# Optimization experiments

Hardware: AMD Instinct MI355X
Metric: run time of the kernel (lower is better)

Reference implementation:

```python
import jax, jax.numpy as jnp
import numpy as np

S, B, C, H, W, N = 2, 16, 80, 128, 128, 128
HW = H * W
EPS = 1e-4
PULL_W = PUSH_W = OFF_W = 1.0


def _sig(x):
    return jnp.clip(jax.nn.sigmoid(x), EPS, 1.0 - EPS)


def _gather_feat(feat, ind):
    # feat [B,C,H,W], ind [B,N] flat HW indices -> [B,N,C]
    b, c = feat.shape[0], feat.shape[1]
    f = feat.transpose(0, 2, 3, 1).reshape(b, -1, c)
    idx = jnp.broadcast_to(ind[:, :, None], (b, ind.shape[1], c))
    return jnp.take_along_axis(f, idx, axis=1)


def _focal(pred, gt):
    pos = gt == 1.0
    neg = gt < 1.0
    negw = jnp.square(jnp.square(1.0 - gt))  # (1-gt)^4
    pos_loss = jnp.sum(jnp.where(pos, jnp.log(pred) * jnp.square(1.0 - pred), 0.0))
    neg_loss = jnp.sum(jnp.where(neg, jnp.log(1.0 - pred) * jnp.square(pred) * negw, 0.0))
    num_pos = jnp.sum(pos.astype(pred.dtype))
    return jnp.where(num_pos > 0, -(pos_loss + neg_loss) / num_pos, -neg_loss)


def _ae(tag0, tag1, mask):
    t0 = tag0[..., 0]  # [B,N]
    t1 = tag1[..., 0]
    m = mask.astype(t0.dtype)
    num = jnp.sum(m, axis=1, keepdims=True)  # [B,1]
    mean = (t0 + t1) * 0.5
    pull = jnp.sum(m * jnp.square(t0 - mean) / (num + EPS)) + \
           jnp.sum(m * jnp.square(t1 - mean) / (num + EPS))
    m2 = m[:, None, :] * m[:, :, None]  # [B,N,N] both-valid pairs
    numc = num[:, :, None]              # [B,1,1]
    num2 = (numc - 1.0) * numc
    dist = jax.nn.relu(1.0 - jnp.abs(mean[:, None, :] - mean[:, :, None]))
    dist = (dist - 1.0 / (numc + EPS)) / (num2 + EPS)
    push = jnp.sum(m2 * dist)
    return pull, push


def _off_loss(off, gt_off, mask):
    m = mask.astype(off.dtype)
    num = jnp.sum(m)
    d = jnp.abs(off - gt_off)
    sl1 = jnp.where(d < 1.0, 0.5 * d * d, d - 0.5)
    return jnp.sum(m[:, :, None] * sl1) / (num + EPS)


def setup_inputs() -> dict:
    key = jax.random.key(0)
    ks = jax.random.split(key, 20)

    def mk_gt(k):
        k1, k2 = jax.random.split(k)
        base = jax.random.uniform(k1, (B, C * H * W), jnp.float32) * 0.99
        idx = jax.random.randint(k2, (B, 64), 0, C * H * W)
        base = base.at[jnp.arange(B)[:, None], idx].set(1.0)
        return base.reshape(B, C, H, W)

    return {
        "tl_heats": jax.random.normal(ks[0], (S, B, C, H, W), jnp.float32),
        "br_heats": jax.random.normal(ks[1], (S, B, C, H, W), jnp.float32),
        "tl_tags": jax.random.normal(ks[2], (S, B, 1, H, W), jnp.float32),
        "br_tags": jax.random.normal(ks[3], (S, B, 1, H, W), jnp.float32),
        "tl_offs": jax.random.normal(ks[4], (S, B, 2, H, W), jnp.float32),
        "br_offs": jax.random.normal(ks[5], (S, B, 2, H, W), jnp.float32),
        "gt_tl_heat": mk_gt(ks[6]),
        "gt_br_heat": mk_gt(ks[7]),
        "gt_tag_mask": jax.random.bernoulli(ks[8], 0.5, (B, N)),
        "gt_off_tl_mask": jax.random.bernoulli(ks[9], 0.5, (B, N)),
        "gt_off_br_mask": jax.random.bernoulli(ks[10], 0.5, (B, N)),
        "gt_tl_off": jax.random.uniform(ks[11], (B, N, 2), jnp.float32),
        "gt_br_off": jax.random.uniform(ks[12], (B, N, 2), jnp.float32),
        "gt_tl_tag_ind": jax.random.randint(ks[13], (B, N), 0, HW),
        "gt_br_tag_ind": jax.random.randint(ks[14], (B, N), 0, HW),
        "gt_tl_off_ind": jax.random.randint(ks[15], (B, N), 0, HW),
        "gt_br_off_ind": jax.random.randint(ks[16], (B, N), 0, HW),
    }


def reference(tl_heats, br_heats, tl_tags, br_tags, tl_offs, br_offs,
              gt_tl_heat, gt_br_heat, gt_tag_mask, gt_off_tl_mask, gt_off_br_mask,
              gt_tl_off, gt_br_off, gt_tl_tag_ind, gt_br_tag_ind,
              gt_tl_off_ind, gt_br_off_ind):
    nstack = tl_heats.shape[0]
    focal = 0.0
    pull = 0.0
    push = 0.0
    off = 0.0
    for s in range(nstack):
        focal = focal + _focal(_sig(tl_heats[s]), gt_tl_heat)
        focal = focal + _focal(_sig(br_heats[s]), gt_br_heat)
        t0 = _gather_feat(tl_tags[s], gt_tl_tag_ind)
        t1 = _gather_feat(br_tags[s], gt_br_tag_ind)
        p, q = _ae(t0, t1, gt_tag_mask)
        pull = pull + p
        push = push + q
        o0 = _gather_feat(tl_offs[s], gt_tl_off_ind)
        o1 = _gather_feat(br_offs[s], gt_br_off_ind)
        off = off + _off_loss(o0, gt_tl_off, gt_off_tl_mask)
        off = off + _off_loss(o1, gt_br_off, gt_off_br_mask)
    loss = (focal + PULL_W * pull + PUSH_W * push + OFF_W * off) / max(nstack, 1)
    return loss[None]
```

## Files before the change

kernel.cpp:

```cpp
#include <hip/hip_runtime.h>
#include <math.h>

constexpr int S_ = 2, B_ = 16, C_ = 80, H_ = 128, W_ = 128, N_ = 128;
constexpr int HW_ = H_ * W_;
constexpr long long BCHW_ = (long long)B_ * C_ * HW_;
constexpr int NV4_ = (int)(BCHW_ / 4);
#define EPSF 1e-4f

constexpr int FOCAL_BPS = 1024;
constexpr int F4_PER_BLOCK = NV4_ / FOCAL_BPS;
constexpr int F4_PER_THREAD = F4_PER_BLOCK / 256;
constexpr int BATCH = 4;
constexpr int NBATCH = F4_PER_THREAD / BATCH;

#define CLAMP_C 9.2102404f


__device__ inline float wave_reduce_sum(float v) {
#pragma unroll
  for (int off = 32; off > 0; off >>= 1) v += __shfl_down(v, off, 64);
  return v;
}

__device__ inline void focal_elem2(float x, float wpos, float wneg, float negw,
                                   float& pacc, float& nacc) {
  float xc = fminf(fmaxf(-x, -CLAMP_C), CLAMP_C);
  float t = __expf(xc);
  float u = 1.0f + t;
  float p = __builtin_amdgcn_rcpf(u);
  float l1 = __logf(u);
  float om = t * p;
  float posv = l1 * om * om;
  float negv = (l1 - xc) * p * p * negw;
  pacc = fmaf(wpos, posv, pacc);
  nacc = fmaf(wneg, negv, nacc);
}

__device__ inline void focal4(const float4& g, const float4& a, const float4& b,
                              float& pacc, float& nacc, float& npos) {
  const float ge[4] = {g.x, g.y, g.z, g.w};
  const float ae[4] = {a.x, a.y, a.z, a.w};
  const float be[4] = {b.x, b.y, b.z, b.w};
#pragma unroll
  for (int k = 0; k < 4; ++k) {
    const float gv = ge[k];
    const float wpos = (gv == 1.0f) ? 1.0f : 0.0f;
    const float wneg = 1.0f - wpos;
    const float omg = 1.0f - gv;
    const float negw = (omg * omg) * (omg * omg);
    npos += wpos;
    focal_elem2(ae[k], wpos, wneg, negw, pacc, nacc);
    focal_elem2(be[k], wpos, wneg, negw, pacc, nacc);
  }
}

__global__ __launch_bounds__(256, 2) void focal_kernel(
    const float4* __restrict__ tl, const float4* __restrict__ br,
    const float4* __restrict__ gtl, const float4* __restrict__ gbr,
    float* __restrict__ ws) {
  const int slice = blockIdx.y;
  const float4* __restrict__ pred = (slice == 0) ? tl : br;
  const float4* __restrict__ gt = (slice == 0) ? gtl : gbr;

  float pacc = 0.0f, nacc = 0.0f, npos = 0.0f;

  const int idx = blockIdx.x * F4_PER_BLOCK + threadIdx.x;

  float4 bg[2][BATCH], ba[2][BATCH], bb[2][BATCH];

#pragma unroll
  for (int i = 0; i < BATCH; ++i) {
    const int j = idx + i * 256;
    bg[0][i] = gt[j];
    ba[0][i] = pred[j];
    bb[0][i] = pred[NV4_ + j];
  }

#pragma unroll
  for (int bt = 0; bt < NBATCH; ++bt) {
    const int cur = bt & 1, nxt = cur ^ 1;
    if (bt + 1 < NBATCH) {
      const int base = idx + (bt + 1) * (BATCH * 256);
#pragma unroll
      for (int i = 0; i < BATCH; ++i) {
        const int j = base + i * 256;
        bg[nxt][i] = gt[j];
        ba[nxt][i] = pred[j];
        bb[nxt][i] = pred[NV4_ + j];
      }
    }
    __builtin_amdgcn_sched_barrier(0);
#pragma unroll
    for (int i = 0; i < BATCH; ++i) {
      focal4(bg[cur][i], ba[cur][i], bb[cur][i], pacc, nacc, npos);
    }
  }

  __shared__ float red[4][3];
  const int wave = threadIdx.x >> 6, lane = threadIdx.x & 63;
  float r0 = wave_reduce_sum(pacc);
  float r1 = wave_reduce_sum(nacc);
  float r2 = wave_reduce_sum(npos);
  if (lane == 0) { red[wave][0] = r0; red[wave][1] = r1; red[wave][2] = r2; }
  __syncthreads();
  if (threadIdx.x == 0) {
    float tp = red[0][0] + red[1][0] + red[2][0] + red[3][0];
    float tn = red[0][1] + red[1][1] + red[2][1] + red[3][1];
    float tc = red[0][2] + red[1][2] + red[2][2] + red[3][2];
    atomicAdd(&ws[0 + slice], tp);
    atomicAdd(&ws[2 + slice], tn);
    atomicAdd(&ws[4 + slice], tc);
  }
}

__device__ inline float sl1f(float d) {
  float a = fabsf(d);
  return (a < 1.0f) ? 0.5f * a * a : a - 0.5f;
}

__global__ __launch_bounds__(128) void ae_off_kernel(
    const float* __restrict__ tl_tags, const float* __restrict__ br_tags,
    const float* __restrict__ tl_offs, const float* __restrict__ br_offs,
    const int* __restrict__ tag_mask,
    const int* __restrict__ off_tl_mask, const int* __restrict__ off_br_mask,
    const float* __restrict__ gt_tl_off, const float* __restrict__ gt_br_off,
    const int* __restrict__ tl_tag_ind, const int* __restrict__ br_tag_ind,
    const int* __restrict__ tl_off_ind, const int* __restrict__ br_off_ind,
    float* __restrict__ ws, float* __restrict__ out) {
  const int s = blockIdx.x / B_;
  const int b = blockIdx.x % B_;
  const int n = threadIdx.x;

  __shared__ float sm_mean[N_];
  __shared__ float sm_m[N_];

  const float m = (tag_mask[b * N_ + n] != 0) ? 1.0f : 0.0f;
  const float t0 = tl_tags[(s * B_ + b) * HW_ + tl_tag_ind[b * N_ + n]];
  const float t1 = br_tags[(s * B_ + b) * HW_ + br_tag_ind[b * N_ + n]];
  const float mean = 0.5f * (t0 + t1);
  sm_mean[n] = mean;
  sm_m[n] = m;
  __syncthreads();

  float num = 0.0f;
  for (int j = 0; j < N_; ++j) num += sm_m[j];
  const float invn = 1.0f / (num + EPSF);
  const float d0 = t0 - mean, d1 = t1 - mean;
  const float pull_n = m * (d0 * d0 + d1 * d1) * invn;

  const float num2 = (num - 1.0f) * num;
  const float inv2 = 1.0f / (num2 + EPSF);
  float pacc = 0.0f;
  for (int j = 0; j < N_; ++j) {
    float dd = 1.0f - fabsf(mean - sm_mean[j]);
    dd = fmaxf(dd, 0.0f);
    pacc += sm_m[j] * (dd - invn);
  }
  const float push_n = m * pacc * inv2;

  const float mo_tl = (off_tl_mask[b * N_ + n] != 0) ? 1.0f : 0.0f;
  const float mo_br = (off_br_mask[b * N_ + n] != 0) ? 1.0f : 0.0f;
  const int io0 = tl_off_ind[b * N_ + n];
  const int io1 = br_off_ind[b * N_ + n];
  const float o00 = tl_offs[((s * B_ + b) * 2 + 0) * HW_ + io0];
  const float o01 = tl_offs[((s * B_ + b) * 2 + 1) * HW_ + io0];
  const float o10 = br_offs[((s * B_ + b) * 2 + 0) * HW_ + io1];
  const float o11 = br_offs[((s * B_ + b) * 2 + 1) * HW_ + io1];
  const float g00 = gt_tl_off[(b * N_ + n) * 2 + 0];
  const float g01 = gt_tl_off[(b * N_ + n) * 2 + 1];
  const float g10 = gt_br_off[(b * N_ + n) * 2 + 0];
  const float g11 = gt_br_off[(b * N_ + n) * 2 + 1];
  const float sl_tl = mo_tl * (sl1f(o00 - g00) + sl1f(o01 - g01));
  const float sl_br = mo_br * (sl1f(o10 - g10) + sl1f(o11 - g11));

  float vals[6] = {pull_n, push_n, sl_tl, sl_br,
                   (s == 0) ? mo_tl : 0.0f, (s == 0) ? mo_br : 0.0f};
  __shared__ float red[2][6];
  const int wave = n >> 6, lane = n & 63;
#pragma unroll
  for (int k = 0; k < 6; ++k) {
    float r = wave_reduce_sum(vals[k]);
    if (lane == 0) red[wave][k] = r;
  }
  __syncthreads();
  if (n == 0) {
    atomicAdd(&ws[10 + s], red[0][0] + red[1][0]);
    atomicAdd(&ws[12 + s], red[0][1] + red[1][1]);
    atomicAdd(&ws[14 + s], red[0][2] + red[1][2]);
    atomicAdd(&ws[16 + s], red[0][3] + red[1][3]);
    atomicAdd(&ws[18], red[0][4] + red[1][4]);
    atomicAdd(&ws[19], red[0][5] + red[1][5]);

    __threadfence();
    unsigned int prev =
        atomicAdd(reinterpret_cast<unsigned int*>(ws + 31), 1u);
    if (prev == (unsigned int)(S_ * B_ - 1)) {
      auto rd = [&](int i) { return atomicAdd(&ws[i], 0.0f); };
      const float npos_tl = rd(4), npos_br = rd(5);
      float focal = 0.0f;
      const float p_tl = rd(0), n_tl = rd(2);
      const float p_br = rd(1), n_br = rd(3);
      focal += (npos_tl > 0.0f) ? (p_tl + n_tl) / npos_tl : n_tl;
      focal += (npos_br > 0.0f) ? (p_br + n_br) / npos_br : n_br;
      const float pull = rd(10) + rd(11);
      const float push = rd(12) + rd(13);
      const float off = (rd(14) + rd(15)) / (rd(18) + EPSF) +
                        (rd(16) + rd(17)) / (rd(19) + EPSF);
      out[0] = (focal + pull + push + off) * 0.5f;
    }
  }
}

extern "C" void kernel_launch(void* const* d_in, const int* in_sizes, int n_in,
                              void* d_out, int out_size, void* d_ws, size_t ws_size,
                              hipStream_t stream) {
  const float* tl_heats   = (const float*)d_in[0];
  const float* br_heats   = (const float*)d_in[1];
  const float* tl_tags    = (const float*)d_in[2];
  const float* br_tags    = (const float*)d_in[3];
  const float* tl_offs    = (const float*)d_in[4];
  const float* br_offs    = (const float*)d_in[5];
  const float* gt_tl_heat = (const float*)d_in[6];
  const float* gt_br_heat = (const float*)d_in[7];
  const int* gt_tag_mask    = (const int*)d_in[8];
  const int* gt_off_tl_mask = (const int*)d_in[9];
  const int* gt_off_br_mask = (const int*)d_in[10];
  const float* gt_tl_off  = (const float*)d_in[11];
  const float* gt_br_off  = (const float*)d_in[12];
  const int* gt_tl_tag_ind = (const int*)d_in[13];
  const int* gt_br_tag_ind = (const int*)d_in[14];
  const int* gt_tl_off_ind = (const int*)d_in[15];
  const int* gt_br_off_ind = (const int*)d_in[16];

  float* ws = (float*)d_ws;
  float* out = (float*)d_out;

  hipMemsetAsync(ws, 0, 32 * sizeof(float), stream);

  dim3 fgrid(FOCAL_BPS, 2, 1);
  focal_kernel<<<fgrid, 256, 0, stream>>>(
      (const float4*)tl_heats, (const float4*)br_heats,
      (const float4*)gt_tl_heat, (const float4*)gt_br_heat, ws);

  ae_off_kernel<<<S_ * B_, N_, 0, stream>>>(
      tl_tags, br_tags, tl_offs, br_offs,
      gt_tag_mask, gt_off_tl_mask, gt_off_br_mask,
      gt_tl_off, gt_br_off,
      gt_tl_tag_ind, gt_br_tag_ind, gt_tl_off_ind, gt_br_off_ind, ws, out);
}
```

Before: 492.8 us.

## Skip positive-term math via wave vote and use base-2 transcendentals in focal kernel

The focal kernel now computes the positive-sample term only when some lane in the wave sees a gt value equal to 1, since positives are very sparse. The exp and log work moves to base-2 hardware intrinsics, and the ln2 scale is applied once in the final combine. Loads become nontemporal, the explicit double-buffer prefetch is replaced by a simple batched loop with BATCH=5, and launch bounds are raised to 4 blocks per CU. This cuts per-element transcendental and ALU work on a memory-bound stream, at the cost of relying on the compiler to overlap loads and possibly using more registers per batch.

```diff
diff --git a/kernel.cpp b/kernel.cpp
--- a/kernel.cpp
+++ b/kernel.cpp
@@ -10,11 +10,19 @@
 constexpr int FOCAL_BPS = 1024;
 constexpr int F4_PER_BLOCK = NV4_ / FOCAL_BPS;
 constexpr int F4_PER_THREAD = F4_PER_BLOCK / 256;
-constexpr int BATCH = 4;
+constexpr int BATCH = 5;
 constexpr int NBATCH = F4_PER_THREAD / BATCH;
 
-#define CLAMP_C 9.2102404f
-
+#define LOG2E 1.4426950408889634f
+#define C2 13.2875677f
+#define LN2F 0.69314718056f
+
+
+typedef float f4v __attribute__((ext_vector_type(4)));
+
+__device__ inline f4v ldnt(const f4v* p) {
+  return __builtin_nontemporal_load(p);
+}
 
 __device__ inline float wave_reduce_sum(float v) {
 #pragma unroll
@@ -22,78 +30,73 @@
   return v;
 }
 
-__device__ inline void focal_elem2(float x, float wpos, float wneg, float negw,
-                                   float& pacc, float& nacc) {
-  float xc = fminf(fmaxf(-x, -CLAMP_C), CLAMP_C);
-  float t = __expf(xc);
+__device__ inline float neg_part(float x) {
+  float z = fminf(fmaxf(x * (-LOG2E), -C2), C2);
+  float t = __builtin_amdgcn_exp2f(z);
   float u = 1.0f + t;
   float p = __builtin_amdgcn_rcpf(u);
-  float l1 = __logf(u);
+  float L = __builtin_amdgcn_logf(u);
+  return (L - z) * (p * p);
+}
+
+__device__ inline float pos_part(float x) {
+  float z = fminf(fmaxf(x * (-LOG2E), -C2), C2);
+  float t = __builtin_amdgcn_exp2f(z);
+  float u = 1.0f + t;
+  float p = __builtin_amdgcn_rcpf(u);
+  float L = __builtin_amdgcn_logf(u);
   float om = t * p;
-  float posv = l1 * om * om;
-  float negv = (l1 - xc) * p * p * negw;
-  pacc = fmaf(wpos, posv, pacc);
-  nacc = fmaf(wneg, negv, nacc);
-}
-
-__device__ inline void focal4(const float4& g, const float4& a, const float4& b,
+  return L * om * om;
+}
+
+__device__ inline void focal4(const f4v g, const f4v a, const f4v b,
                               float& pacc, float& nacc, float& npos) {
-  const float ge[4] = {g.x, g.y, g.z, g.w};
-  const float ae[4] = {a.x, a.y, a.z, a.w};
-  const float be[4] = {b.x, b.y, b.z, b.w};
+  float mx = fmaxf(fmaxf(g[0], g[1]), fmaxf(g[2], g[3]));
 #pragma unroll
   for (int k = 0; k < 4; ++k) {
-    const float gv = ge[k];
-    const float wpos = (gv == 1.0f) ? 1.0f : 0.0f;
-    const float wneg = 1.0f - wpos;
-    const float omg = 1.0f - gv;
-    const float negw = (omg * omg) * (omg * omg);
-    npos += wpos;
-    focal_elem2(ae[k], wpos, wneg, negw, pacc, nacc);
-    focal_elem2(be[k], wpos, wneg, negw, pacc, nacc);
-  }
-}
-
-__global__ __launch_bounds__(256, 2) void focal_kernel(
-    const float4* __restrict__ tl, const float4* __restrict__ br,
-    const float4* __restrict__ gtl, const float4* __restrict__ gbr,
+    float gv = g[k];
+    float omg = 1.0f - gv;
+    float o2 = omg * omg;
+    float negw = o2 * o2;
+    nacc = fmaf(neg_part(a[k]), negw, nacc);
+    nacc = fmaf(neg_part(b[k]), negw, nacc);
+  }
+  if (__any(mx == 1.0f)) {
+#pragma unroll
+    for (int k = 0; k < 4; ++k) {
+      float wpos = (g[k] == 1.0f) ? 1.0f : 0.0f;
+      npos += wpos;
+      pacc = fmaf(wpos, pos_part(a[k]) + pos_part(b[k]), pacc);
+    }
+  }
+}
+
+__global__ __launch_bounds__(256, 4) void focal_kernel(
+    const f4v* __restrict__ tl, const f4v* __restrict__ br,
+    const f4v* __restrict__ gtl, const f4v* __restrict__ gbr,
     float* __restrict__ ws) {
   const int slice = blockIdx.y;
-  const float4* __restrict__ pred = (slice == 0) ? tl : br;
-  const float4* __restrict__ gt = (slice == 0) ? gtl : gbr;
+  const f4v* __restrict__ pred = (slice == 0) ? tl : br;
+  const f4v* __restrict__ gt = (slice == 0) ? gtl : gbr;
 
   float pacc = 0.0f, nacc = 0.0f, npos = 0.0f;
 
-  const int idx = blockIdx.x * F4_PER_BLOCK + threadIdx.x;
-
-  float4 bg[2][BATCH], ba[2][BATCH], bb[2][BATCH];
-
-#pragma unroll
-  for (int i = 0; i < BATCH; ++i) {
-    const int j = idx + i * 256;
-    bg[0][i] = gt[j];
-    ba[0][i] = pred[j];
-    bb[0][i] = pred[NV4_ + j];
-  }
-
-#pragma unroll
+  int idx = blockIdx.x * F4_PER_BLOCK + threadIdx.x;
+
   for (int bt = 0; bt < NBATCH; ++bt) {
-    const int cur = bt & 1, nxt = cur ^ 1;
-    if (bt + 1 < NBATCH) {
-      const int base = idx + (bt + 1) * (BATCH * 256);
-#pragma unroll
-      for (int i = 0; i < BATCH; ++i) {
-        const int j = base + i * 256;
-        bg[nxt][i] = gt[j];
-        ba[nxt][i] = pred[j];
-        bb[nxt][i] = pred[NV4_ + j];
-      }
-    }
-    __builtin_amdgcn_sched_barrier(0);
+    f4v g[BATCH], a[BATCH], b[BATCH];
 #pragma unroll
     for (int i = 0; i < BATCH; ++i) {
-      focal4(bg[cur][i], ba[cur][i], bb[cur][i], pacc, nacc, npos);
-    }
+      const int j = idx + i * 256;
+      g[i] = ldnt(gt + j);
+      a[i] = ldnt(pred + j);
+      b[i] = ldnt(pred + NV4_ + j);
+    }
+#pragma unroll
+    for (int i = 0; i < BATCH; ++i) {
+      focal4(g[i], a[i], b[i], pacc, nacc, npos);
+    }
+    idx += BATCH * 256;
   }
 
   __shared__ float red[4][3];
@@ -198,8 +201,8 @@
       auto rd = [&](int i) { return atomicAdd(&ws[i], 0.0f); };
       const float npos_tl = rd(4), npos_br = rd(5);
       float focal = 0.0f;
-      const float p_tl = rd(0), n_tl = rd(2);
-      const float p_br = rd(1), n_br = rd(3);
+      const float p_tl = rd(0) * LN2F, n_tl = rd(2) * LN2F;
+      const float p_br = rd(1) * LN2F, n_br = rd(3) * LN2F;
       focal += (npos_tl > 0.0f) ? (p_tl + n_tl) / npos_tl : n_tl;
       focal += (npos_br > 0.0f) ? (p_br + n_br) / npos_br : n_br;
       const float pull = rd(10) + rd(11);
@@ -239,8 +242,8 @@
 
   dim3 fgrid(FOCAL_BPS, 2, 1);
   focal_kernel<<<fgrid, 256, 0, stream>>>(
-      (const float4*)tl_heats, (const float4*)br_heats,
-      (const float4*)gt_tl_heat, (const float4*)gt_br_heat, ws);
+      (const f4v*)tl_heats, (const f4v*)br_heats,
+      (const f4v*)gt_tl_heat, (const f4v*)gt_br_heat, ws);
 
   ae_off_kernel<<<S_ * B_, N_, 0, stream>>>(
       tl_tags, br_tags, tl_offs, br_offs,
```

New measurement: 566.3 us. 1.15x slower.
